# Performance work log

Hardware: AMD Instinct MI355X
Metric: run time of the kernel (lower is better)

Reference implementation:

```python
import jax, jax.numpy as jnp
import numpy as np

D_MODEL = 1024
NUM_HEAD = 16
D_HEAD = 64
SEQ = 1024
MEM = 1024
BATCH = 4
LN_EPS = 1e-5


def _rel_shift(x):
    # x: [i, j, b, n] -- Transformer-XL relative shift trick
    i, j, b, n = x.shape
    zero_pad = jnp.zeros((i, 1, b, n), dtype=x.dtype)
    x_padded = jnp.concatenate([zero_pad, x], axis=1).reshape(j + 1, i, b, n)
    return x_padded[1:].reshape(i, j, b, n)


def setup_inputs() -> dict:
    key = jax.random.key(0)
    ks = jax.random.split(key, 8)
    w_scale = 1.0 / np.sqrt(D_MODEL)  # keep activations O(1)
    total = MEM + SEQ
    return {
        "x": jax.random.normal(ks[0], (SEQ, BATCH, D_MODEL), jnp.float32),
        "memory": jax.random.normal(ks[1], (MEM, BATCH, D_MODEL), jnp.float32),
        "pos_emb": jax.random.normal(ks[2], (total, BATCH, D_MODEL), jnp.float32),
        "pos_bias_u": jax.random.normal(ks[3], (NUM_HEAD, D_HEAD), jnp.float32) * 0.02,
        "pos_bias_v": jax.random.normal(ks[4], (NUM_HEAD, D_HEAD), jnp.float32) * 0.02,
        "W_qkv": jax.random.normal(ks[5], (3 * NUM_HEAD * D_HEAD, D_MODEL), jnp.float32) * w_scale,
        "W_rel": jax.random.normal(ks[6], (NUM_HEAD * D_HEAD, D_MODEL), jnp.float32) * w_scale,
        "W_o": jax.random.normal(ks[7], (D_MODEL, NUM_HEAD * D_HEAD), jnp.float32) * w_scale,
        "ln_gamma": jnp.ones((D_MODEL,), jnp.float32),
        "ln_beta": jnp.zeros((D_MODEL,), jnp.float32),
    }


def reference(x, memory, pos_emb, pos_bias_u, pos_bias_v, W_qkv, W_rel, W_o, ln_gamma, ln_beta):
    seq_len = x.shape[0]
    c = jnp.concatenate([memory, x], axis=0)        # [T, B, D]
    T, B = c.shape[0], c.shape[1]
    n, d = pos_bias_u.shape
    scale = 1.0 / np.sqrt(d)

    heads = c @ W_qkv.T                              # [T, B, 3*n*d]
    q, k, v = jnp.split(heads, 3, axis=-1)
    q = q.reshape(T, B, n, d)[-seq_len:]             # [S, B, n, d]
    k = k.reshape(T, B, n, d)                        # [T, B, n, d]
    v = v.reshape(T, B, n, d)
    r = (pos_emb @ W_rel.T).reshape(T, B, n, d)      # [T, B, n, d]

    AC = jnp.einsum('ibnd,jbnd->ijbn', q + pos_bias_u, k)
    BD = _rel_shift(jnp.einsum('ibnd,jbnd->ijbn', q + pos_bias_v, r))
    attn_score = (AC + BD) * scale                   # [S, T, B, n]
    attn_prob = jax.nn.softmax(attn_score, axis=1)   # softmax over key dim (dropout = eval identity)

    attn_vec = jnp.einsum('ijbn,jbnd->ibnd', attn_prob, v).reshape(seq_len, B, n * d)
    attn_out = attn_vec @ W_o.T                      # [S, B, D]

    y = x + attn_out
    mu = jnp.mean(y, axis=-1, keepdims=True)
    var = jnp.mean(jnp.square(y - mu), axis=-1, keepdims=True)
    return ln_gamma * (y - mu) / jnp.sqrt(var + LN_EPS) + ln_beta
```

## Files before the change

### kernel.cpp

```cpp
#include <hip/hip_runtime.h>

#define S_ 1024
#define M_ 1024
#define T_ 2048
#define B_ 4
#define H_ 16
#define DM_ 1024
#define DH_ 64

typedef __attribute__((ext_vector_type(8))) short s16x8;
typedef __attribute__((ext_vector_type(16))) float f32x16;

__device__ __forceinline__ unsigned short f2b(float x){
  unsigned int u = __float_as_uint(x);
  u = (u + 0x7fffu + ((u>>16)&1u)) >> 16;
  return (unsigned short)u;
}
__device__ __forceinline__ float b2f(unsigned short h){
  return __uint_as_float(((unsigned int)h)<<16);
}
__device__ __forceinline__ uint4 pack8(const float* v){
  uint4 o;
  o.x = (unsigned)f2b(v[0]) | ((unsigned)f2b(v[1])<<16);
  o.y = (unsigned)f2b(v[2]) | ((unsigned)f2b(v[3])<<16);
  o.z = (unsigned)f2b(v[4]) | ((unsigned)f2b(v[5])<<16);
  o.w = (unsigned)f2b(v[6]) | ((unsigned)f2b(v[7])<<16);
  return o;
}
__device__ __forceinline__ void glds16(const unsigned short* g, unsigned short* l){
  __builtin_amdgcn_global_load_lds((const __attribute__((address_space(1))) void*)g,
                                   (__attribute__((address_space(3))) void*)l, 16, 0, 0);
}

#define BAR_L()  asm volatile("s_waitcnt lgkmcnt(0)\ns_barrier" ::: "memory")
#define BAR_VL() asm volatile("s_waitcnt vmcnt(0) lgkmcnt(0)\ns_barrier" ::: "memory")

__global__ __launch_bounds__(256) void cast_all(
    const float* __restrict__ mem, const float* __restrict__ x,
    const float* __restrict__ pos, const float* __restrict__ wqkv,
    const float* __restrict__ wrel, const float* __restrict__ wo,
    unsigned short* __restrict__ c16, unsigned short* __restrict__ pos16,
    unsigned short* __restrict__ wq16, unsigned short* __restrict__ wr16,
    unsigned short* __restrict__ wo16)
{
  int u = blockIdx.x*256 + threadIdx.x;
  const float* s; unsigned short* d;
  if (u < 1048576)      { s = (u < 524288) ? mem + (size_t)u*8 : x + (size_t)(u-524288)*8;
                          d = c16 + (size_t)u*8; }
  else if (u < 2097152) { int v = u - 1048576; s = pos  + (size_t)v*8; d = pos16 + (size_t)v*8; }
  else if (u < 2490368) { int v = u - 2097152; s = wqkv + (size_t)v*8; d = wq16  + (size_t)v*8; }
  else if (u < 2621440) { int v = u - 2490368; s = wrel + (size_t)v*8; d = wr16  + (size_t)v*8; }
  else                  { int v = u - 2621440; s = wo   + (size_t)v*8; d = wo16  + (size_t)v*8; }
  float4 x0 = *(const float4*)s;
  float4 x1 = *(const float4*)(s+4);
  float f[8] = {x0.x,x0.y,x0.z,x0.w,x1.x,x1.y,x1.z,x1.w};
  *(uint4*)d = pack8(f);
}

__global__ __launch_bounds__(256) void gemm_nt(const unsigned short* __restrict__ A,
    const unsigned short* __restrict__ Bw, void* __restrict__ Cout,
    const float* __restrict__ res, int Ntot, int K, int mode)
{
  __shared__ __align__(16) unsigned short a_s[128*64];
  __shared__ __align__(16) unsigned short b_s[128*64];
  const int tid = threadIdx.x;
  const int lane = tid & 63, wave = tid >> 6;
  const int wr = wave >> 1, wc = wave & 1;
  const long m0 = (long)blockIdx.y * 128, n0 = (long)blockIdx.x * 128;
  f32x16 acc[2][2];
  for (int qa=0;qa<2;qa++) for(int qb=0;qb<2;qb++) for (int e=0;e<16;e++) acc[qa][qb][e]=0.f;
  int srow[4], scol[4];
  for (int c = 0; c < 4; c++) {
    int ch = c*256 + tid;
    srow[c] = ch >> 3;
    scol[c] = (((ch & 7) ^ (srow[c] & 7))) * 8;
  }
  for (int k0 = 0; k0 < K; k0 += 64) {
    for (int c = 0; c < 4; c++) {
      int ch = c*256 + tid;
      glds16(&A[(size_t)(m0+srow[c])*K + k0 + scol[c]], &a_s[ch*8]);
      glds16(&Bw[(size_t)(n0+srow[c])*K + k0 + scol[c]], &b_s[ch*8]);
    }
    __syncthreads();
    for (int ks = 0; ks < 4; ks++) {
      const int kb = ks*2 + (lane>>5);
      s16x8 af[2], bf[2];
      for (int q = 0; q < 2; q++) {
        int ra = wr*64 + q*32 + (lane&31);
        int rb = wc*64 + q*32 + (lane&31);
        af[q] = *(const s16x8*)&a_s[ra*64 + ((kb ^ (ra&7))<<3)];
        bf[q] = *(const s16x8*)&b_s[rb*64 + ((kb ^ (rb&7))<<3)];
      }
      for (int qr=0;qr<2;qr++)
        for (int qc2=0;qc2<2;qc2++)
          acc[qr][qc2] = __builtin_amdgcn_mfma_f32_32x32x16_bf16(af[qr], bf[qc2], acc[qr][qc2], 0,0,0);
    }
    __syncthreads();
  }
  for (int qr=0;qr<2;qr++)
    for (int qc2=0;qc2<2;qc2++)
      for (int e=0;e<16;e++){
        long row = m0 + wr*64 + qr*32 + (e&3) + 8*(e>>2) + 4*(lane>>5);
        long col = n0 + wc*64 + qc2*32 + (lane&31);
        size_t o = (size_t)row*Ntot + col;
        if (mode == 0) ((unsigned short*)Cout)[o] = f2b(acc[qr][qc2][e]);
        else           ((float*)Cout)[o] = acc[qr][qc2][e] + res[o];
      }
}

__global__ __launch_bounds__(256) void scatter_quv(const unsigned short* __restrict__ qkvo,
   const float* __restrict__ u, const float* __restrict__ v,
   unsigned short* __restrict__ QU, unsigned short* __restrict__ QV)
{
  int gid = blockIdx.x*256 + threadIdx.x;
  int d0 = (gid & 7) * 8;
  int i  = (gid >> 3) & (S_-1);
  int bh = gid >> 13;
  int b = bh >> 4, h = bh & 15;
  size_t src = (size_t)((M_+i)*B_ + b)*3072 + h*64 + d0;
  uint4 q8 = *(const uint4*)&qkvo[src];
  float f[8];
  f[0]=b2f(q8.x&0xffff); f[1]=b2f(q8.x>>16); f[2]=b2f(q8.y&0xffff); f[3]=b2f(q8.y>>16);
  f[4]=b2f(q8.z&0xffff); f[5]=b2f(q8.z>>16); f[6]=b2f(q8.w&0xffff); f[7]=b2f(q8.w>>16);
  float fu[8], fv[8];
  for (int e=0;e<8;e++){ fu[e] = f[e] + u[h*64+d0+e]; fv[e] = f[e] + v[h*64+d0+e]; }
  size_t dst = ((size_t)bh*S_ + i)*64 + d0;
  *(uint4*)&QU[dst] = pack8(fu);
  *(uint4*)&QV[dst] = pack8(fv);
}

__global__ __launch_bounds__(256) void scatter_vt(const unsigned short* __restrict__ qkvo,
    unsigned short* __restrict__ VT)
{
  __shared__ __align__(16) unsigned short v_s[64*72];
  const int tid = threadIdx.x;
  const int bh = blockIdx.x, b = bh>>4, h = bh&15;
  const int t0 = blockIdx.y*64;
  const unsigned short* Vg = qkvo + (size_t)b*3072 + 2048 + h*64;
  for (int c=0;c<2;c++){
    int ch = c*256 + tid;
    int r = ch>>3, off = (ch&7)*8;
    *(uint4*)&v_s[r*72+off] = *(const uint4*)&Vg[(size_t)(t0+r)*12288 + off];
  }
  __syncthreads();
  for (int c=0;c<2;c++){
    int ch = c*256 + tid;
    int d = ch>>3, toff = (ch&7)*8;
    unsigned short vals[8];
    for (int e=0;e<8;e++) vals[e] = v_s[(toff+e)*72 + d];
    uint4 pk;
    pk.x = (unsigned)vals[0] | ((unsigned)vals[1]<<16);
    pk.y = (unsigned)vals[2] | ((unsigned)vals[3]<<16);
    pk.z = (unsigned)vals[4] | ((unsigned)vals[5]<<16);
    pk.w = (unsigned)vals[6] | ((unsigned)vals[7]<<16);
    *(uint4*)&VT[((size_t)bh*64 + d)*T_ + t0 + toff] = pk;
  }
}

__global__ __launch_bounds__(256,2) void flash_attn4(
    const unsigned short* __restrict__ QU, const unsigned short* __restrict__ QV,
    const unsigned short* __restrict__ qkvo, const unsigned short* __restrict__ VT,
    const unsigned short* __restrict__ relo, unsigned short* __restrict__ AV)
{
  __shared__ __align__(16) unsigned short qu_s[64*72];
  __shared__ __align__(16) unsigned short qv_s[65*72];
  __shared__ __align__(16) unsigned short k_s [64*64];
  __shared__ __align__(16) unsigned short vt_s[2][64*64];
  __shared__ __align__(16) unsigned short rg_s[128*64];
  __shared__ __align__(16) unsigned short p_s [64*72];
  __shared__ float l_s[64];

  const int tid = threadIdx.x, lane = tid&63, wave = tid>>6;
  const int bh = blockIdx.x, b = bh>>4, h = bh&15;
  const int i0 = blockIdx.y*64;
  const int qr = wave>>1, qc = wave&1;
  const int hi = lane>>5, ll = lane&31;
  const unsigned short* QUb = QU + (size_t)bh*S_*DH_;
  const unsigned short* QVb = QV + (size_t)bh*S_*DH_;
  const unsigned short* Kg  = qkvo + (size_t)b*3072 + 1024 + h*64;
  const unsigned short* VTb = VT + (size_t)bh*64*T_;
  const unsigned short* Rg  = relo + (size_t)b*1024 + h*64;

  const int s0r = tid>>3,        s0c = (((tid&7)       ^ (s0r&7)))*8;
  const int s1r = (256+tid)>>3,  s1c = ((((256+tid)&7) ^ (s1r&7)))*8;

  int vb = 0;

  glds16(&Kg [(size_t)(0+s0r)*12288 + s0c], &k_s[(size_t)tid*8]);
  glds16(&Kg [(size_t)(0+s1r)*12288 + s1c], &k_s[(size_t)(256+tid)*8]);
  glds16(&VTb[(size_t)s0r*T_ + 0 + s0c],    &vt_s[0][(size_t)tid*8]);
  glds16(&VTb[(size_t)s1r*T_ + 0 + s1c],    &vt_s[0][(size_t)(256+tid)*8]);
  {
    const int wb0 = 0 - i0 + 960;
    for (int c=0;c<4;c++){
      int ch = c*256+tid; int rr = ch>>3, off = ch&7;
      int t = wb0 + rr; t = t < 0 ? 0 : (t > T_-1 ? T_-1 : t);
      int sc = ((off ^ (rr&7)))*8;
      glds16(&Rg[(size_t)t*4096 + sc], &rg_s[(size_t)ch*8]);
    }
  }
  for (int c=0;c<2;c++){
    int ch = c*256+tid; int row = ch>>3, off=(ch&7)*8;
    *(uint4*)&qu_s[row*72+off] = *(const uint4*)&QUb[(size_t)(i0+row)*64 + off];
    *(uint4*)&qv_s[row*72+off] = *(const uint4*)&QVb[(size_t)(i0+row)*64 + off];
  }
  if (tid < 8) {
    int rr = i0 + 64; if (rr > S_-1) rr = S_-1;
    *(uint4*)&qv_s[64*72 + tid*8] = *(const uint4*)&QVb[(size_t)rr*64 + tid*8];
  }
  BAR_L();

  s16x8 qur0, qur1, qur2, qur3;
  s16x8 qv00, qv01, qv02, qv03;
  {
    const int ro = (qr*32+ll)*72 + hi*8;
    qur0 = *(const s16x8*)&qu_s[ro +  0];
    qur1 = *(const s16x8*)&qu_s[ro + 16];
    qur2 = *(const s16x8*)&qu_s[ro + 32];
    qur3 = *(const s16x8*)&qu_s[ro + 48];
    qv00 = *(const s16x8*)&qv_s[ro +  0];
    qv01 = *(const s16x8*)&qv_s[ro + 16];
    qv02 = *(const s16x8*)&qv_s[ro + 32];
    qv03 = *(const s16x8*)&qv_s[ro + 48];
  }

  s16x8 ones;
  for (int e=0;e<8;e++) ones[e] = (short)0x3F80;

  f32x16 acc_o, acc_l;
  for (int e=0;e<16;e++){ acc_o[e]=0.f; acc_l[e]=0.f; }

  const int col = qc*32 + ll;
  const int cbase = (qc - qr + 1) * 32;

  for (int j0 = 0; j0 < T_; j0 += 64) {
    const int jdmax = j0 + 63 - i0;
    const int jdmin = j0 - 63 - i0;
    const int cls = (jdmax <= 1024) ? 0 : ((jdmin >= 1026) ? 2 : 1);
    const int jn = j0 + 64;

    BAR_VL();

    if (jn < T_) {
      glds16(&VTb[(size_t)s0r*T_ + jn + s0c], &vt_s[vb^1][(size_t)tid*8]);
      glds16(&VTb[(size_t)s1r*T_ + jn + s1c], &vt_s[vb^1][(size_t)(256+tid)*8]);
    }

    s16x8 av0, av1, av2, av3;
    if (cls == 2) {
      const int ro1 = (qr*32+ll+1)*72 + hi*8;
      av0 = *(const s16x8*)&qv_s[ro1 +  0];
      av1 = *(const s16x8*)&qv_s[ro1 + 16];
      av2 = *(const s16x8*)&qv_s[ro1 + 32];
      av3 = *(const s16x8*)&qv_s[ro1 + 48];
    } else {
      av0 = qv00; av1 = qv01; av2 = qv02; av3 = qv03;
    }

    f32x16 gacc0, gacc1;
    for (int e=0;e<16;e++){ gacc0[e]=0.f; gacc1[e]=0.f; }
    __builtin_amdgcn_s_setprio(1);
#define BANDK(KS, AV) { \
      int kb = KS*2 + hi; \
      { int br = cbase + ll; \
        s16x8 bb = *(const s16x8*)&rg_s[br*64 + ((kb ^ (br&7))<<3)]; \
        gacc0 = __builtin_amdgcn_mfma_f32_32x32x16_bf16(AV, bb, gacc0, 0,0,0); } \
      { int br = cbase + 32 + ll; \
        s16x8 bb = *(const s16x8*)&rg_s[br*64 + ((kb ^ (br&7))<<3)]; \
        gacc1 = __builtin_amdgcn_mfma_f32_32x32x16_bf16(AV, bb, gacc1, 0,0,0); } }
    BANDK(0, av0) BANDK(1, av1) BANDK(2, av2) BANDK(3, av3)

    f32x16 acc;
    for (int e=0;e<16;e++) acc[e]=0.f;
#define ACK(KS, AU) { \
      int kb = KS*2 + hi; \
      int rbk = qc*32 + ll; \
      s16x8 bq = *(const s16x8*)&k_s[rbk*64 + ((kb ^ (rbk&7))<<3)]; \
      acc = __builtin_amdgcn_mfma_f32_32x32x16_bf16(AU, bq, acc, 0,0,0); }
    ACK(0, qur0) ACK(1, qur1) ACK(2, qur2) ACK(3, qur3)
    __builtin_amdgcn_s_setprio(0);
    BAR_L();

    if (jn < T_) {
      glds16(&Kg[(size_t)(jn+s0r)*12288 + s0c], &k_s[(size_t)tid*8]);
      glds16(&Kg[(size_t)(jn+s1r)*12288 + s1c], &k_s[(size_t)(256+tid)*8]);
      if (cls != 1) {
        const int jdmaxn = jn + 63 - i0;
        const int jdminn = jn - 63 - i0;
        const int clsn = (jdmaxn <= 1024) ? 0 : ((jdminn >= 1026) ? 2 : 1);
        const int wbn = (clsn == 2) ? (jn - i0 - 1089) : (jn - i0 + 960);
        for (int c=0;c<4;c++){
          int ch = c*256+tid; int rr = ch>>3, off = ch&7;
          int t = wbn + rr; t = t < 0 ? 0 : (t > T_-1 ? T_-1 : t);
          int sc = ((off ^ (rr&7)))*8;
          glds16(&Rg[(size_t)t*4096 + sc], &rg_s[(size_t)ch*8]);
        }
      }
    }

    for (int e=0;e<16;e++){
      int rm = 4*hi + (e&3) + 8*(e>>2);
      int r  = qr*32 + rm;
      int jd = j0 + col - (i0 + r);
      int li = ((((ll - rm + 31) & 31) | (hi<<5)) << 2);
      float g0 = __uint_as_float((unsigned)__builtin_amdgcn_ds_bpermute(li, (int)__float_as_uint(gacc0[e])));
      float g1 = __uint_as_float((unsigned)__builtin_amdgcn_ds_bpermute(li, (int)__float_as_uint(gacc1[e])));
      float bd = (ll > rm) ? g1 : g0;
      if (jd == 1025) bd = 0.f;
      float p = __expf((acc[e] + bd) * 0.125f);
      if (!(cls == 1 && jd >= 1026)) p_s[r*72 + col] = f2b(p);
    }

    if (cls == 1) {
      const int wb2 = j0 - i0 - 1089;
      for (int c=0;c<4;c++){
        int ch = c*256+tid; int rr = ch>>3, off = ch&7;
        int t = wb2 + rr; t = t < 0 ? 0 : (t > T_-1 ? T_-1 : t);
        int sc = ((off ^ (rr&7)))*8;
        glds16(&Rg[(size_t)t*4096 + sc], &rg_s[(size_t)ch*8]);
      }
      BAR_VL();
      f32x16 g2a, g2b;
      for (int e=0;e<16;e++){ g2a[e]=0.f; g2b[e]=0.f; }
      __builtin_amdgcn_s_setprio(1);
#define BANDW(KS) { \
        int kb = KS*2 + hi; \
        const int ro1 = (qr*32+ll+1)*72 + hi*8; \
        s16x8 a = *(const s16x8*)&qv_s[ro1 + KS*16]; \
        { int br = cbase + ll; \
          s16x8 bb = *(const s16x8*)&rg_s[br*64 + ((kb ^ (br&7))<<3)]; \
          g2a = __builtin_amdgcn_mfma_f32_32x32x16_bf16(a, bb, g2a, 0,0,0); } \
        { int br = cbase + 32 + ll; \
          s16x8 bb = *(const s16x8*)&rg_s[br*64 + ((kb ^ (br&7))<<3)]; \
          g2b = __builtin_amdgcn_mfma_f32_32x32x16_bf16(a, bb, g2b, 0,0,0); } }
      BANDW(0) BANDW(1) BANDW(2) BANDW(3)
      __builtin_amdgcn_s_setprio(0);
      for (int e=0;e<16;e++){
        int rm = 4*hi + (e&3) + 8*(e>>2);
        int r  = qr*32 + rm;
        int jd = j0 + col - (i0 + r);
        int li = ((((ll - rm + 31) & 31) | (hi<<5)) << 2);
        float g0 = __uint_as_float((unsigned)__builtin_amdgcn_ds_bpermute(li, (int)__float_as_uint(g2a[e])));
        float g1 = __uint_as_float((unsigned)__builtin_amdgcn_ds_bpermute(li, (int)__float_as_uint(g2b[e])));
        float bd = (ll > rm) ? g1 : g0;
        float p = __expf((acc[e] + bd) * 0.125f);
        if (jd >= 1026) p_s[r*72 + col] = f2b(p);
      }
      BAR_L();
      if (jn < T_) {
        const int jdmaxn = jn + 63 - i0;
        const int jdminn = jn - 63 - i0;
        const int clsn = (jdmaxn <= 1024) ? 0 : ((jdminn >= 1026) ? 2 : 1);
        const int wbn = (clsn == 2) ? (jn - i0 - 1089) : (jn - i0 + 960);
        for (int c=0;c<4;c++){
          int ch = c*256+tid; int rr = ch>>3, off = ch&7;
          int t = wbn + rr; t = t < 0 ? 0 : (t > T_-1 ? T_-1 : t);
          int sc = ((off ^ (rr&7)))*8;
          glds16(&Rg[(size_t)t*4096 + sc], &rg_s[(size_t)ch*8]);
        }
      }
    } else {
      BAR_L();
    }

    __builtin_amdgcn_s_setprio(1);
    for (int ks=0; ks<4; ks++){
      int koff = ks*16 + hi*8, kb = ks*2 + hi;
      int rbv = qc*32 + ll;
      s16x8 a  = *(const s16x8*)&p_s[(qr*32+ll)*72 + koff];
      s16x8 bv = *(const s16x8*)&vt_s[vb][rbv*64 + ((kb ^ (rbv&7))<<3)];
      acc_o = __builtin_amdgcn_mfma_f32_32x32x16_bf16(a, bv, acc_o, 0,0,0);
      acc_l = __builtin_amdgcn_mfma_f32_32x32x16_bf16(a, ones, acc_l, 0,0,0);
    }
    __builtin_amdgcn_s_setprio(0);
    vb ^= 1;
  }

  if (qc == 0 && ll == 0) {
    for (int e=0;e<16;e++){
      int r = qr*32 + 4*hi + (e&3) + 8*(e>>2);
      l_s[r] = acc_l[e];
    }
  }
  BAR_L();
  for (int e=0;e<16;e++){
    int r = qr*32 + 4*hi + (e&3) + 8*(e>>2);
    float oo = acc_o[e] / l_s[r];
    AV[ ((size_t)(i0+r)*B_ + b)*(H_*DH_) + h*DH_ + col ] = f2b(oo);
  }
#undef BANDK
#undef ACK
#undef BANDW
}

__global__ __launch_bounds__(256) void ln_kernel(const float* __restrict__ y,
    const float* __restrict__ g, const float* __restrict__ be, float* __restrict__ o)
{
  __shared__ float red[8];
  int row = blockIdx.x, tid = threadIdx.x;
  const float* yr = y + (size_t)row*DM_;
  float v[4];
  for (int e=0;e<4;e++) v[e] = yr[tid + 256*e];
  float s = v[0]+v[1]+v[2]+v[3];
  for (int off=32; off>0; off>>=1) s += __shfl_down(s, off, 64);
  if ((tid&63)==0) red[tid>>6] = s;
  __syncthreads();
  if (tid==0) red[4] = red[0]+red[1]+red[2]+red[3];
  __syncthreads();
  float mu = red[4] * (1.f/DM_);
  __syncthreads();
  float q = 0.f;
  for (int e=0;e<4;e++){ float d = v[e]-mu; q += d*d; }
  for (int off=32; off>0; off>>=1) q += __shfl_down(q, off, 64);
  if ((tid&63)==0) red[tid>>6] = q;
  __syncthreads();
  if (tid==0) red[4] = red[0]+red[1]+red[2]+red[3];
  __syncthreads();
  float rstd = rsqrtf(red[4]*(1.f/DM_) + 1e-5f);
  for (int e=0;e<4;e++){
    int c = tid + 256*e;
    o[(size_t)row*DM_ + c] = g[c]*(v[e]-mu)*rstd + be[c];
  }
}

extern "C" void kernel_launch(void* const* d_in, const int* in_sizes, int n_in,
                              void* d_out, int out_size, void* d_ws, size_t ws_size,
                              hipStream_t stream)
{
  const float* x    = (const float*)d_in[0];
  const float* mem  = (const float*)d_in[1];
  const float* pos  = (const float*)d_in[2];
  const float* pbu  = (const float*)d_in[3];
  const float* pbv  = (const float*)d_in[4];
  const float* wqkv = (const float*)d_in[5];
  const float* wrel = (const float*)d_in[6];
  const float* wo   = (const float*)d_in[7];
  const float* gam  = (const float*)d_in[8];
  const float* bet  = (const float*)d_in[9];
  float* out = (float*)d_out;

  char* w = (char*)d_ws;
  unsigned short* qkvo  = (unsigned short*)(w + 0);
  unsigned short* relo  = (unsigned short*)(w + 50331648);
  unsigned short* wo16  = (unsigned short*)(w + 67108864);
  unsigned short* QUb   = (unsigned short*)(w + 69206016);
  unsigned short* QVb   = (unsigned short*)(w + 77594624);
  unsigned short* VT    = (unsigned short*)(w + 85983232);
  unsigned short* av16  = (unsigned short*)(w + 102760448);
  float*          yf    = (float*)(w + 111149056);
  unsigned short* c16   = (unsigned short*)(w + 127926272);
  unsigned short* pos16 = (unsigned short*)(w + 144703488);
  unsigned short* wq16  = (unsigned short*)(w + 161480704);
  unsigned short* wr16  = (unsigned short*)(w + 167772160);

  cast_all<<<10752, 256, 0, stream>>>(mem, x, pos, wqkv, wrel, wo,
                                      c16, pos16, wq16, wr16, wo16);

  gemm_nt<<<dim3(24,64), 256, 0, stream>>>(c16,   wq16, (void*)qkvo, nullptr, 3072, 1024, 0);
  gemm_nt<<<dim3(8,64),  256, 0, stream>>>(pos16, wr16, (void*)relo, nullptr, 1024, 1024, 0);

  scatter_quv<<<2048, 256, 0, stream>>>(qkvo, pbu, pbv, QUb, QVb);
  scatter_vt<<<dim3(64,32), 256, 0, stream>>>(qkvo, VT);

  flash_attn4<<<dim3(64,16), 256, 0, stream>>>(QUb, QVb, qkvo, VT, relo, av16);

  gemm_nt<<<dim3(8,32), 256, 0, stream>>>(av16, wo16, (void*)yf, x, 1024, 1024, 1);
  ln_kernel<<<4096, 256, 0, stream>>>(yf, gam, bet, out);
}
```

Baseline: 508.3 us.

## Shrink attention LDS footprint to fit three blocks per CU

Drops the qu_s buffer by staging QU through p_s, which now uses an XOR-swizzled 64-wide layout instead of 72-wide padding. It also turns the V tile into a single buffer loaded at the start of each iteration rather than prefetched one tile ahead. Launch bounds move from 2 to 3 blocks per CU to use the freed LDS for occupancy. Separately, the rel-shift path selects gacc0 or gacc1 before a single ds_bpermute, halving the permutes. The cost is that the V load is no longer overlapped with the previous tile's compute, and register pressure under the tighter bound may cause spills.

```diff
diff --git a/kernel.cpp b/kernel.cpp
--- a/kernel.cpp
+++ b/kernel.cpp
@@ -157,17 +157,16 @@
   }
 }
 
-__global__ __launch_bounds__(256,2) void flash_attn4(
+__global__ __launch_bounds__(256,3) void flash_attn4(
     const unsigned short* __restrict__ QU, const unsigned short* __restrict__ QV,
     const unsigned short* __restrict__ qkvo, const unsigned short* __restrict__ VT,
     const unsigned short* __restrict__ relo, unsigned short* __restrict__ AV)
 {
-  __shared__ __align__(16) unsigned short qu_s[64*72];
   __shared__ __align__(16) unsigned short qv_s[65*72];
   __shared__ __align__(16) unsigned short k_s [64*64];
-  __shared__ __align__(16) unsigned short vt_s[2][64*64];
+  __shared__ __align__(16) unsigned short vt_s[64*64];
   __shared__ __align__(16) unsigned short rg_s[128*64];
-  __shared__ __align__(16) unsigned short p_s [64*72];
+  __shared__ __align__(16) unsigned short p_s [64*64];
   __shared__ float l_s[64];
 
   const int tid = threadIdx.x, lane = tid&63, wave = tid>>6;
@@ -184,12 +183,8 @@
   const int s0r = tid>>3,        s0c = (((tid&7)       ^ (s0r&7)))*8;
   const int s1r = (256+tid)>>3,  s1c = ((((256+tid)&7) ^ (s1r&7)))*8;
 
-  int vb = 0;
-
   glds16(&Kg [(size_t)(0+s0r)*12288 + s0c], &k_s[(size_t)tid*8]);
   glds16(&Kg [(size_t)(0+s1r)*12288 + s1c], &k_s[(size_t)(256+tid)*8]);
-  glds16(&VTb[(size_t)s0r*T_ + 0 + s0c],    &vt_s[0][(size_t)tid*8]);
-  glds16(&VTb[(size_t)s1r*T_ + 0 + s1c],    &vt_s[0][(size_t)(256+tid)*8]);
   {
     const int wb0 = 0 - i0 + 960;
     for (int c=0;c<4;c++){
@@ -200,9 +195,9 @@
     }
   }
   for (int c=0;c<2;c++){
-    int ch = c*256+tid; int row = ch>>3, off=(ch&7)*8;
-    *(uint4*)&qu_s[row*72+off] = *(const uint4*)&QUb[(size_t)(i0+row)*64 + off];
-    *(uint4*)&qv_s[row*72+off] = *(const uint4*)&QVb[(size_t)(i0+row)*64 + off];
+    int ch = c*256+tid; int row = ch>>3, off=(ch&7);
+    *(uint4*)&p_s[row*64 + ((off ^ (row&7))<<3)] = *(const uint4*)&QUb[(size_t)(i0+row)*64 + off*8];
+    *(uint4*)&qv_s[row*72+off*8] = *(const uint4*)&QVb[(size_t)(i0+row)*64 + off*8];
   }
   if (tid < 8) {
     int rr = i0 + 64; if (rr > S_-1) rr = S_-1;
@@ -213,16 +208,18 @@
   s16x8 qur0, qur1, qur2, qur3;
   s16x8 qv00, qv01, qv02, qv03;
   {
-    const int ro = (qr*32+ll)*72 + hi*8;
-    qur0 = *(const s16x8*)&qu_s[ro +  0];
-    qur1 = *(const s16x8*)&qu_s[ro + 16];
-    qur2 = *(const s16x8*)&qu_s[ro + 32];
-    qur3 = *(const s16x8*)&qu_s[ro + 48];
+    const int rq = qr*32 + ll;
+    qur0 = *(const s16x8*)&p_s[rq*64 + (((0*2+hi) ^ (rq&7))<<3)];
+    qur1 = *(const s16x8*)&p_s[rq*64 + (((1*2+hi) ^ (rq&7))<<3)];
+    qur2 = *(const s16x8*)&p_s[rq*64 + (((2*2+hi) ^ (rq&7))<<3)];
+    qur3 = *(const s16x8*)&p_s[rq*64 + (((3*2+hi) ^ (rq&7))<<3)];
+    const int ro = rq*72 + hi*8;
     qv00 = *(const s16x8*)&qv_s[ro +  0];
     qv01 = *(const s16x8*)&qv_s[ro + 16];
     qv02 = *(const s16x8*)&qv_s[ro + 32];
     qv03 = *(const s16x8*)&qv_s[ro + 48];
   }
+  BAR_VL();
 
   s16x8 ones;
   for (int e=0;e<8;e++) ones[e] = (short)0x3F80;
@@ -239,12 +236,10 @@
     const int cls = (jdmax <= 1024) ? 0 : ((jdmin >= 1026) ? 2 : 1);
     const int jn = j0 + 64;
 
-    BAR_VL();
-
-    if (jn < T_) {
-      glds16(&VTb[(size_t)s0r*T_ + jn + s0c], &vt_s[vb^1][(size_t)tid*8]);
-      glds16(&VTb[(size_t)s1r*T_ + jn + s1c], &vt_s[vb^1][(size_t)(256+tid)*8]);
-    }
+    BAR_L();
+
+    glds16(&VTb[(size_t)s0r*T_ + j0 + s0c], &vt_s[(size_t)tid*8]);
+    glds16(&VTb[(size_t)s1r*T_ + j0 + s1c], &vt_s[(size_t)(256+tid)*8]);
 
     s16x8 av0, av1, av2, av3;
     if (cls == 2) {
@@ -302,13 +297,14 @@
       int rm = 4*hi + (e&3) + 8*(e>>2);
       int r  = qr*32 + rm;
       int jd = j0 + col - (i0 + r);
+      int tl = (ll + rm + 1) & 31;
+      float sel = (tl > rm) ? gacc1[e] : gacc0[e];
       int li = ((((ll - rm + 31) & 31) | (hi<<5)) << 2);
-      float g0 = __uint_as_float((unsigned)__builtin_amdgcn_ds_bpermute(li, (int)__float_as_uint(gacc0[e])));
-      float g1 = __uint_as_float((unsigned)__builtin_amdgcn_ds_bpermute(li, (int)__float_as_uint(gacc1[e])));
-      float bd = (ll > rm) ? g1 : g0;
+      float bd = __uint_as_float((unsigned)__builtin_amdgcn_ds_bpermute(li, (int)__float_as_uint(sel)));
       if (jd == 1025) bd = 0.f;
       float p = __expf((acc[e] + bd) * 0.125f);
-      if (!(cls == 1 && jd >= 1026)) p_s[r*72 + col] = f2b(p);
+      if (!(cls == 1 && jd >= 1026))
+        p_s[r*64 + (((col>>3) ^ (r&7))<<3) + (col&7)] = f2b(p);
     }
 
     if (cls == 1) {
@@ -339,12 +335,13 @@
         int rm = 4*hi + (e&3) + 8*(e>>2);
         int r  = qr*32 + rm;
         int jd = j0 + col - (i0 + r);
+        int tl = (ll + rm + 1) & 31;
+        float sel = (tl > rm) ? g2b[e] : g2a[e];
         int li = ((((ll - rm + 31) & 31) | (hi<<5)) << 2);
-        float g0 = __uint_as_float((unsigned)__builtin_amdgcn_ds_bpermute(li, (int)__float_as_uint(g2a[e])));
-        float g1 = __uint_as_float((unsigned)__builtin_amdgcn_ds_bpermute(li, (int)__float_as_uint(g2b[e])));
-        float bd = (ll > rm) ? g1 : g0;
+        float bd = __uint_as_float((unsigned)__builtin_amdgcn_ds_bpermute(li, (int)__float_as_uint(sel)));
         float p = __expf((acc[e] + bd) * 0.125f);
-        if (jd >= 1026) p_s[r*72 + col] = f2b(p);
+        if (jd >= 1026)
+          p_s[r*64 + (((col>>3) ^ (r&7))<<3) + (col&7)] = f2b(p);
       }
       BAR_L();
       if (jn < T_) {
@@ -359,21 +356,20 @@
           glds16(&Rg[(size_t)t*4096 + sc], &rg_s[(size_t)ch*8]);
         }
       }
-    } else {
-      BAR_L();
-    }
+    }
+
+    BAR_VL();
 
     __builtin_amdgcn_s_setprio(1);
     for (int ks=0; ks<4; ks++){
-      int koff = ks*16 + hi*8, kb = ks*2 + hi;
-      int rbv = qc*32 + ll;
-      s16x8 a  = *(const s16x8*)&p_s[(qr*32+ll)*72 + koff];
-      s16x8 bv = *(const s16x8*)&vt_s[vb][rbv*64 + ((kb ^ (rbv&7))<<3)];
+      int kb = ks*2 + hi;
+      int rv = qr*32 + ll, rbv = qc*32 + ll;
+      s16x8 a  = *(const s16x8*)&p_s[rv*64 + ((kb ^ (rv&7))<<3)];
+      s16x8 bv = *(const s16x8*)&vt_s[rbv*64 + ((kb ^ (rbv&7))<<3)];
       acc_o = __builtin_amdgcn_mfma_f32_32x32x16_bf16(a, bv, acc_o, 0,0,0);
       acc_l = __builtin_amdgcn_mfma_f32_32x32x16_bf16(a, ones, acc_l, 0,0,0);
     }
     __builtin_amdgcn_s_setprio(0);
-    vb ^= 1;
   }
 
   if (qc == 0 && ll == 0) {
```

New measurement: 771.6 us. 51.8% more time.
